# Kernel optimization log

Measured on AMD Instinct MI355X. Metric: run time of the kernel, lower is better.

## Reference

```python
import jax, jax.numpy as jnp
import numpy as np

B, G, D = 256, 14, 2048          # batch, grid, vis_embed_dim
H, A, SI, WI, ST = 1024, 512, 1024, 1024, 256  # sent_hidden, att, sent_input, word_input, int_stop
T = 10                           # max_no_of_sent


def _lin(key, out_d, in_d):
    k1, k2 = jax.random.split(key)
    return (jax.random.normal(k1, (out_d, in_d), jnp.float32) * 0.02,
            jax.random.normal(k2, (out_d,), jnp.float32) * 0.02)


def setup_inputs() -> dict:
    key = jax.random.key(0)
    ks = jax.random.split(key, 14)
    inp = {}
    inp['vis_enc_output'] = jax.random.normal(ks[0], (B, G, G, D), jnp.float32)
    inp['captions'] = jax.random.randint(ks[1], (B, T, 20), 0, 1000, jnp.int64 if jax.config.jax_enable_x64 else jnp.int32)
    inp['enc_att_w'], inp['enc_att_b'] = _lin(ks[2], A, D)
    inp['dec_att_w'], inp['dec_att_b'] = _lin(ks[3], A, H)
    inp['full_att_w'], inp['full_att_b'] = _lin(ks[4], 1, A)
    inp['ctx_w'], inp['ctx_b'] = _lin(ks[5], SI, D)
    inp['w_ih'], inp['b_ih'] = _lin(ks[6], 4 * H, SI)
    inp['w_hh'], inp['b_hh'] = _lin(ks[7], 4 * H, H)
    inp['topic_h_w'], inp['topic_h_b'] = _lin(ks[8], WI, H)
    inp['topic_c_w'], inp['topic_c_b'] = _lin(ks[9], WI, SI)
    inp['stop_p_w'], inp['stop_p_b'] = _lin(ks[10], ST, H)
    inp['stop_c_w'], inp['stop_c_b'] = _lin(ks[11], ST, H)
    inp['final_w'], inp['final_b'] = _lin(ks[12], 2, ST)
    return inp


def _forward(vis_enc_output, captions, enc_att_w, enc_att_b, dec_att_w, dec_att_b,
             full_att_w, full_att_b, ctx_w, ctx_b, w_ih, b_ih, w_hh, b_hh,
             topic_h_w, topic_h_b, topic_c_w, topic_c_b,
             stop_p_w, stop_p_b, stop_c_w, stop_c_b, final_w, final_b):
    bsz = vis_enc_output.shape[0]
    v = vis_enc_output.reshape(bsz, -1, vis_enc_output.shape[-1])  # [B, N, D]
    n_sent = captions.shape[1]
    # encoder projection is hoisted out of the loop (same math each step)
    enc_proj = jnp.einsum('bnd,ad->bna', v, enc_att_w) + enc_att_b  # [B, N, A]
    hdim = w_hh.shape[1]

    def step(carry, _):
        h, c = carry
        dec = h @ dec_att_w.T + dec_att_b                            # [B, A]
        join = jnp.tanh(enc_proj + dec[:, None, :])                  # [B, N, A]
        logits = join @ full_att_w[0] + full_att_b[0]                # [B, N]
        scores = jax.nn.softmax(logits, axis=1)
        att_out = jnp.einsum('bn,bnd->bd', scores, v)                # [B, D]
        ctx = att_out @ ctx_w.T + ctx_b                              # [B, SI]
        h_prev = h
        gates = ctx @ w_ih.T + b_ih + h @ w_hh.T + b_hh              # [B, 4H]
        i, f, g, o = jnp.split(gates, 4, axis=1)
        c_new = jax.nn.sigmoid(f) * c + jax.nn.sigmoid(i) * jnp.tanh(g)
        h_new = jax.nn.sigmoid(o) * jnp.tanh(c_new)
        topic = jnp.tanh(h_new @ topic_h_w.T + topic_h_b + ctx @ topic_c_w.T + topic_c_b)
        p = jnp.tanh(h_prev @ stop_p_w.T + stop_p_b + h_new @ stop_c_w.T + stop_c_b)
        p = p @ final_w.T + final_b                                  # [B, 2]
        return (h_new, c_new), (topic, p)

    h0 = jnp.zeros((bsz, hdim), v.dtype)
    c0 = jnp.zeros((bsz, hdim), v.dtype)
    (_, _), (topics, ps) = jax.lax.scan(step, (h0, c0), None, length=n_sent)
    return topics.transpose(1, 0, 2), ps.transpose(1, 0, 2)  # [B, T, WI], [B, T, 2]


def reference(vis_enc_output, captions, enc_att_w, enc_att_b, dec_att_w, dec_att_b,
              full_att_w, full_att_b, ctx_w, ctx_b, w_ih, b_ih, w_hh, b_hh,
              topic_h_w, topic_h_b, topic_c_w, topic_c_b,
              stop_p_w, stop_p_b, stop_c_w, stop_c_b, final_w, final_b):
    return _forward(vis_enc_output, captions, enc_att_w, enc_att_b, dec_att_w, dec_att_b,
                    full_att_w, full_att_b, ctx_w, ctx_b, w_ih, b_ih, w_hh, b_hh,
                    topic_h_w, topic_h_b, topic_c_w, topic_c_b,
                    stop_p_w, stop_p_b, stop_c_w, stop_c_b, final_w, final_b)
```

## Files before the change

kernel.cpp:

```cpp
#include <hip/hip_runtime.h>
#include <cstdint>

#define B_   256
#define NPOS 196
#define D_   2048
#define H_   1024
#define A_   512
#define T_   10

#define N13  6144
#define OFF_DEC    0
#define OFF_WHH    512
#define OFF_STOPP  4608
#define OFF_TOPICH 4864
#define OFF_STOPC  5888
#define NC   5120

#define QMAX 6.5f
#define QSINV (127.f / QMAX)
#define QS    (QMAX / 127.f)

#define PS13 ((size_t)B_ * N13)
#define PSNC ((size_t)B_ * NC)

typedef __attribute__((ext_vector_type(8))) short bf16x8;
typedef __attribute__((ext_vector_type(4))) short bf16x4;
typedef __attribute__((ext_vector_type(4))) float f32x4;

__device__ __forceinline__ float b2f(short s) {
  union { unsigned int u; float f; } c;
  c.u = ((unsigned int)(unsigned short)s) << 16;
  return c.f;
}
__device__ __forceinline__ short f2b(float f) {
  union { float f; unsigned int u; } c; c.f = f;
  unsigned int u = c.u + 0x7fffu + ((c.u >> 16) & 1u);
  return (short)(u >> 16);
}
__device__ __forceinline__ float fast_tanh(float x) {
  float a = fabsf(x);
  float e = __expf(-2.f * a);
  float t = __fdividef(1.f - e, 1.f + e);
  return x < 0.f ? -t : t;
}
__device__ __forceinline__ float fast_sigm(float x) {
  return __fdividef(1.f, 1.f + __expf(-x));
}

#define GLDS16(g, l) __builtin_amdgcn_global_load_lds( \
    (const __attribute__((address_space(1))) void*)(g), \
    (__attribute__((address_space(3))) void*)(l), 16, 0, 0)

__global__ __launch_bounds__(256) void cvtq_v_k(
    const float* __restrict__ in, short* __restrict__ v16,
    unsigned char* __restrict__ v8, long n)
{
  long i = ((long)blockIdx.x * blockDim.x + threadIdx.x) * 8;
  const long stride = (long)gridDim.x * blockDim.x * 8;
  for (; i < n; i += stride) {
    float4 a = *(const float4*)(in + i);
    float4 b = *(const float4*)(in + i + 4);
    bf16x8 o;
    o[0]=f2b(a.x); o[1]=f2b(a.y); o[2]=f2b(a.z); o[3]=f2b(a.w);
    o[4]=f2b(b.x); o[5]=f2b(b.y); o[6]=f2b(b.z); o[7]=f2b(b.w);
    *(bf16x8*)(v16 + i) = o;
    float v[8] = {a.x,a.y,a.z,a.w,b.x,b.y,b.z,b.w};
    unsigned int w0 = 0, w1 = 0;
    #pragma unroll
    for (int j = 0; j < 4; ++j) {
      float q = fminf(fmaxf(rintf(v[j] * QSINV), -127.f), 127.f) + 128.f;
      w0 |= ((unsigned int)(int)q) << (8 * j);
    }
    #pragma unroll
    for (int j = 0; j < 4; ++j) {
      float q = fminf(fmaxf(rintf(v[4+j] * QSINV), -127.f), 127.f) + 128.f;
      w1 |= ((unsigned int)(int)q) << (8 * j);
    }
    uint2 pk; pk.x = w0; pk.y = w1;
    *(uint2*)(v8 + i) = pk;
  }
}

__global__ void cvt_k(const float* __restrict__ in, short* __restrict__ out, long n)
{
  long i = ((long)blockIdx.x * blockDim.x + threadIdx.x) * 8;
  const long stride = (long)gridDim.x * blockDim.x * 8;
  for (; i < n; i += stride) {
    float4 a = *(const float4*)(in + i);
    float4 b = *(const float4*)(in + i + 4);
    bf16x8 o;
    o[0]=f2b(a.x); o[1]=f2b(a.y); o[2]=f2b(a.z); o[3]=f2b(a.w);
    o[4]=f2b(b.x); o[5]=f2b(b.y); o[6]=f2b(b.z); o[7]=f2b(b.w);
    *(bf16x8*)(out + i) = o;
  }
}

struct SegTab {
  const float* src[8];
  short* dst[8];
  int cum[9];
};
__global__ __launch_bounds__(256) void cvt_multi_k(SegTab t)
{
  int seg = 0;
  #pragma unroll
  for (int s = 0; s < 7; ++s) seg += (int)(blockIdx.x >= (unsigned)t.cum[s + 1]);
  const long i = ((long)(blockIdx.x - t.cum[seg]) * 256 + threadIdx.x) * 8;
  const float* in = t.src[seg];
  float4 a = *(const float4*)(in + i);
  float4 b = *(const float4*)(in + i + 4);
  bf16x8 o;
  o[0]=f2b(a.x); o[1]=f2b(a.y); o[2]=f2b(a.z); o[3]=f2b(a.w);
  o[4]=f2b(b.x); o[5]=f2b(b.y); o[6]=f2b(b.z); o[7]=f2b(b.w);
  *(bf16x8*)(t.dst[seg] + i) = o;
}

__global__ __launch_bounds__(256) void transpose_cvt_k(
    const float* __restrict__ in, short* __restrict__ out, int R, int C)
{
  __shared__ float t[32][33];
  const int r0 = blockIdx.y * 32, c0 = blockIdx.x * 32;
  const int tx = threadIdx.x & 31, ty = threadIdx.x >> 5;
  #pragma unroll
  for (int i = 0; i < 32; i += 8)
    t[ty + i][tx] = in[(size_t)(r0 + ty + i) * C + c0 + tx];
  __syncthreads();
  #pragma unroll
  for (int i = 0; i < 32; i += 8)
    out[(size_t)(c0 + ty + i) * R + r0 + tx] = f2b(t[tx][ty + i]);
}

__global__ __launch_bounds__(256) void biasc_k(
    const float* __restrict__ w_ih, const float* __restrict__ b_ih,
    const float* __restrict__ topic_c_w, const float* __restrict__ topic_c_b,
    const float* __restrict__ ctx_b, float* __restrict__ out)
{
  const int r = blockIdx.x * 4 + (threadIdx.x >> 6);
  const int l = threadIdx.x & 63;
  const float* wr; float bb;
  if (r < 4096) { wr = w_ih + (size_t)r * 1024;               bb = b_ih[r]; }
  else          { wr = topic_c_w + (size_t)(r - 4096) * 1024; bb = topic_c_b[r - 4096]; }
  float s = 0.f;
  #pragma unroll
  for (int k = 0; k < 16; ++k) s += wr[l + 64 * k] * ctx_b[l + 64 * k];
  #pragma unroll
  for (int o = 32; o; o >>= 1) s += __shfl_down(s, o);
  if (!l) out[r] = s + bb;
}

__global__ __launch_bounds__(256) void bias13_k(
    const float* __restrict__ dec_att_b, const float* __restrict__ b_hh,
    const float* __restrict__ stop_p_b, const float* __restrict__ topic_h_b,
    const float* __restrict__ stop_c_b, float* __restrict__ bias13)
{
  const int j = blockIdx.x * 256 + threadIdx.x;
  float v;
  if      (j < OFF_WHH)    v = dec_att_b[j];
  else if (j < OFF_STOPP)  v = b_hh[j - OFF_WHH];
  else if (j < OFF_TOPICH) v = stop_p_b[j - OFF_STOPP];
  else if (j < OFF_STOPC)  v = topic_h_b[j - OFF_TOPICH];
  else                     v = stop_c_b[j - OFF_STOPC];
  bias13[j] = v;
}

template<int OUTBF16, int BN, int SWZ, int KZ>
__global__ __launch_bounds__(256) void gemm_bt_k(
    const short* __restrict__ Aptr, const short* __restrict__ Bptr,
    const float* __restrict__ bias, void* __restrict__ Cout,
    int M, int N, int K)
{
  constexpr int TOT = 16 + BN / 8;
  constexpr int NW  = BN / 32;
  __shared__ short As[128 * 64];
  __shared__ short Bs[BN * 64];
  const int tid = threadIdx.x;
  const int l = tid & 63, wv = tid >> 6;
  const int wr = wv >> 1, wc = wv & 1;
  size_t m0, n0;
  if (SWZ) {
    const int id  = blockIdx.y * 4 + blockIdx.x;
    const int xcd = id & 7, s = id >> 3;
    m0 = (size_t)(xcd * 49 + (s >> 2)) * 128;
    n0 = (size_t)(s & 3) * BN;
  } else {
    m0 = (size_t)blockIdx.y * 128;
    n0 = (size_t)blockIdx.x * BN;
  }
  const int srow = l >> 3, scol = (l & 7) * 8;
  const int lr = l & 15, lg = l >> 4;
  const int KC = K / KZ;
  const int kbase = (KZ > 1) ? blockIdx.z * KC : 0;

  f32x4 acc[4][NW];
  #pragma unroll
  for (int i = 0; i < 4; ++i)
    #pragma unroll
    for (int j = 0; j < NW; ++j) acc[i][j] = (f32x4){0.f, 0.f, 0.f, 0.f};

  for (int k0 = kbase; k0 < kbase + KC; k0 += 64) {
    #pragma unroll
    for (int i = 0; i < TOT / 4; ++i) {
      const int c = i * 4 + wv;
      if (c < 16) {
        const int row = c * 8 + srow;
        GLDS16(Aptr + (m0 + row) * (size_t)K + k0 + scol, As + c * 512);
      } else {
        const int row = (c - 16) * 8 + srow;
        GLDS16(Bptr + (n0 + row) * (size_t)K + k0 + scol, Bs + (c - 16) * 512);
      }
    }
    __syncthreads();
    #pragma unroll
    for (int kk = 0; kk < 64; kk += 32) {
      bf16x8 af[4], bfr[NW];
      #pragma unroll
      for (int m = 0; m < 4; ++m)
        af[m] = *(const bf16x8*)(As + (wr * 64 + m * 16 + lr) * 64 + kk + lg * 8);
      #pragma unroll
      for (int n = 0; n < NW; ++n)
        bfr[n] = *(const bf16x8*)(Bs + (wc * (BN / 2) + n * 16 + lr) * 64 + kk + lg * 8);
      #pragma unroll
      for (int m = 0; m < 4; ++m)
        #pragma unroll
        for (int n = 0; n < NW; ++n)
          acc[m][n] = __builtin_amdgcn_mfma_f32_16x16x32_bf16(af[m], bfr[n], acc[m][n], 0, 0, 0);
    }
    __syncthreads();
  }

  #pragma unroll
  for (int m = 0; m < 4; ++m) {
    const size_t row = m0 + wr * 64 + m * 16 + lg * 4;
    #pragma unroll
    for (int n = 0; n < NW; ++n) {
      const size_t col = n0 + wc * (BN / 2) + n * 16 + lr;
      if (KZ > 1) {
        float* Cp = (float*)Cout + (size_t)blockIdx.z * M * (size_t)N;
        #pragma unroll
        for (int r = 0; r < 4; ++r)
          Cp[(row + r) * (size_t)N + col] = acc[m][n][r];
      } else {
        const float bv = bias[col];
        #pragma unroll
        for (int r = 0; r < 4; ++r) {
          const float v = acc[m][n][r] + bv;
          if (OUTBF16) ((short*)Cout)[(row + r) * (size_t)N + col] = f2b(v);
          else         ((float*)Cout)[(row + r) * (size_t)N + col] = v;
        }
      }
    }
  }
}

template<int DO_FINAL, int DO_SCORES>
__global__ __launch_bounds__(512) void sf_k(
    const float* __restrict__ pcur, const float* __restrict__ pprev,
    const float* __restrict__ g3p, const float* __restrict__ biasc,
    const float* __restrict__ bias13,
    const short* __restrict__ encp, const float* __restrict__ fullw,
    const float* __restrict__ finw, const float* __restrict__ finb,
    float* __restrict__ scbuf, float* __restrict__ out_t,
    float* __restrict__ out_p, int tprev)
{
  const int b = blockIdx.x, tid = threadIdx.x;
  const int l = tid & 63, wv = tid >> 6;
  const size_t b13 = (size_t)b * N13;
  __shared__ float dec_s[A_], fw_s[A_], sc[NPOS], red[16], pp[256];

  if (DO_FINAL) {
    float* ot = out_t + (size_t)b * (T_ * 1024) + (size_t)tprev * 1024;
    #pragma unroll
    for (int i = 0; i < 2; ++i) {
      const int j = tid + i * 512;
      float th = bias13[OFF_TOPICH + j] + pcur[b13 + OFF_TOPICH + j]
               + pcur[PS13 + b13 + OFF_TOPICH + j];
      float tc = biasc[4096 + j];
      #pragma unroll
      for (int z = 0; z < 4; ++z) tc += g3p[z * PSNC + (size_t)b * NC + 4096 + j];
      ot[j] = fast_tanh(th + tc);
    }
    if (tid < 256) {
      float a = bias13[OFF_STOPP + tid] + pprev[b13 + OFF_STOPP + tid]
              + pprev[PS13 + b13 + OFF_STOPP + tid];
      float c = bias13[OFF_STOPC + tid] + pcur[b13 + OFF_STOPC + tid]
              + pcur[PS13 + b13 + OFF_STOPC + tid];
      pp[tid] = fast_tanh(a + c);
    }
  }
  if (DO_SCORES && tid < A_) {
    dec_s[tid] = pcur[b13 + tid] + pcur[PS13 + b13 + tid] + bias13[tid];
    fw_s[tid]  = fullw[tid];
  }
  __syncthreads();

  if (DO_FINAL && wv < 2) {
    float s = 0.f;
    #pragma unroll
    for (int k = 0; k < 4; ++k) s += pp[l + 64 * k] * finw[wv * 256 + l + 64 * k];
    #pragma unroll
    for (int o = 32; o; o >>= 1) s += __shfl_down(s, o);
    if (!l) out_p[(size_t)b * (T_ * 2) + tprev * 2 + wv] = s + finb[wv];
  }

  if (DO_SCORES) {
    const short* ep = encp + (size_t)b * NPOS * A_;
    for (int n = wv; n < NPOS; n += 8) {
      bf16x8 e = *(const bf16x8*)(ep + (size_t)n * A_ + l * 8);
      float s = 0.f;
      #pragma unroll
      for (int j = 0; j < 8; ++j)
        s += fast_tanh(b2f(e[j]) + dec_s[l * 8 + j]) * fw_s[l * 8 + j];
      #pragma unroll
      for (int o = 32; o; o >>= 1) s += __shfl_down(s, o);
      if (!l) sc[n] = s;
    }
    __syncthreads();

    float lm = (tid < NPOS) ? sc[tid] : -3e38f;
    #pragma unroll
    for (int o = 32; o; o >>= 1) lm = fmaxf(lm, __shfl_down(lm, o));
    if (!l) red[wv] = lm;
    __syncthreads();
    float mx = red[0];
    #pragma unroll
    for (int i = 1; i < 8; ++i) mx = fmaxf(mx, red[i]);
    const float ev = (tid < NPOS) ? __expf(sc[tid] - mx) : 0.f;
    float es = ev;
    #pragma unroll
    for (int o = 32; o; o >>= 1) es += __shfl_down(es, o);
    if (!l) red[8 + wv] = es;
    __syncthreads();
    float tot = red[8];
    #pragma unroll
    for (int i = 1; i < 8; ++i) tot += red[8 + i];
    if (tid < NPOS) scbuf[(size_t)b * NPOS + tid] = ev * __fdividef(1.f, tot);
  }
}

template<int VMODE>
__global__ __launch_bounds__(256) void pv_k(
    const void* __restrict__ vptr, const float* __restrict__ scbuf,
    short* __restrict__ attout)
{
  const int b = blockIdx.y;
  const int dbase = blockIdx.x * 1024;
  const int tid = threadIdx.x;
  const int grp = tid >> 7;
  const int dt = (tid & 127) * 8;
  __shared__ float sc[NPOS];
  __shared__ float tmp[1024];
  if (tid < NPOS) sc[tid] = scbuf[(size_t)b * NPOS + tid];
  __syncthreads();

  float a[8] = {0,0,0,0,0,0,0,0};
  if (VMODE == 1) {
    const unsigned char* vb = (const unsigned char*)vptr
        + (size_t)b * NPOS * D_ + dbase + dt;
    #pragma unroll 8
    for (int n = grp; n < NPOS; n += 2) {
      const float s = sc[n];
      const uint2 w = *(const uint2*)(vb + (size_t)n * D_);
      a[0] += s * (float)(w.x & 255u);
      a[1] += s * (float)((w.x >> 8) & 255u);
      a[2] += s * (float)((w.x >> 16) & 255u);
      a[3] += s * (float)(w.x >> 24);
      a[4] += s * (float)(w.y & 255u);
      a[5] += s * (float)((w.y >> 8) & 255u);
      a[6] += s * (float)((w.y >> 16) & 255u);
      a[7] += s * (float)(w.y >> 24);
    }
  } else {
    const float* vf = (const float*)vptr + (size_t)b * NPOS * D_ + dbase + dt;
    #pragma unroll 2
    for (int n = grp; n < NPOS; n += 2) {
      const float s = sc[n];
      float4 v0 = *(const float4*)(vf + (size_t)n * D_);
      float4 v1 = *(const float4*)(vf + (size_t)n * D_ + 4);
      a[0] += s*v0.x; a[1] += s*v0.y; a[2] += s*v0.z; a[3] += s*v0.w;
      a[4] += s*v1.x; a[5] += s*v1.y; a[6] += s*v1.z; a[7] += s*v1.w;
    }
  }
  if (grp == 1) {
    #pragma unroll
    for (int j = 0; j < 8; ++j) tmp[dt + j] = a[j];
  }
  __syncthreads();
  if (grp == 0) {
    bf16x8 o8;
    #pragma unroll
    for (int j = 0; j < 8; ++j) {
      float v = a[j] + tmp[dt + j];
      if (VMODE == 1) v = v * QS - 128.f * QS;
      o8[j] = f2b(v);
    }
    *(bf16x8*)(attout + (size_t)b * D_ + dbase + dt) = o8;
  }
}

__global__ __launch_bounds__(256) void lstm_k(
    const float* __restrict__ g3p, const float* __restrict__ gPp,
    const float* __restrict__ biasc, const float* __restrict__ bias13,
    float* __restrict__ c, short* __restrict__ hbf)
{
  const int idx = (blockIdx.x * 256 + threadIdx.x) * 4;
  const int b = idx >> 10, j = idx & 1023;
  f32x4 gate[4];
  #pragma unroll
  for (int g = 0; g < 4; ++g) {
    const size_t base  = (size_t)b * NC + g * 1024 + j;
    const size_t baseh = (size_t)b * N13 + OFF_WHH + g * 1024 + j;
    f32x4 s = *(const f32x4*)(biasc + g * 1024 + j);
    s += *(const f32x4*)(bias13 + OFF_WHH + g * 1024 + j);
    #pragma unroll
    for (int z = 0; z < 4; ++z) s += *(const f32x4*)(g3p + z * PSNC + base);
    #pragma unroll
    for (int z = 0; z < 2; ++z) s += *(const f32x4*)(gPp + z * PS13 + baseh);
    gate[g] = s;
  }
  f32x4 cv = *(const f32x4*)(c + idx);
  f32x4 cn;
  bf16x4 hn;
  #pragma unroll
  for (int k = 0; k < 4; ++k) {
    const float nc2 = fast_sigm(gate[1][k]) * cv[k]
                    + fast_sigm(gate[0][k]) * fast_tanh(gate[2][k]);
    cn[k] = nc2;
    hn[k] = f2b(fast_sigm(gate[3][k]) * fast_tanh(nc2));
  }
  *(f32x4*)(c + idx) = cn;
  *(bf16x4*)(hbf + idx) = hn;
}

extern "C" void kernel_launch(void* const* d_in, const int* in_sizes, int n_in,
                              void* d_out, int out_size, void* d_ws, size_t ws_size,
                              hipStream_t stream)
{
  const float* vis       = (const float*)d_in[0];
  const float* enc_att_w = (const float*)d_in[2];
  const float* enc_att_b = (const float*)d_in[3];
  const float* dec_att_w = (const float*)d_in[4];
  const float* dec_att_b = (const float*)d_in[5];
  const float* full_att_w= (const float*)d_in[6];
  const float* ctx_w     = (const float*)d_in[8];
  const float* ctx_b     = (const float*)d_in[9];
  const float* w_ih      = (const float*)d_in[10];
  const float* b_ih      = (const float*)d_in[11];
  const float* w_hh      = (const float*)d_in[12];
  const float* b_hh      = (const float*)d_in[13];
  const float* topic_h_w = (const float*)d_in[14];
  const float* topic_h_b = (const float*)d_in[15];
  const float* topic_c_w = (const float*)d_in[16];
  const float* topic_c_b = (const float*)d_in[17];
  const float* stop_p_w  = (const float*)d_in[18];
  const float* stop_p_b  = (const float*)d_in[19];
  const float* stop_c_w  = (const float*)d_in[20];
  const float* stop_c_b  = (const float*)d_in[21];
  const float* final_w   = (const float*)d_in[22];
  const float* final_b   = (const float*)d_in[23];

  uint8_t* wsp = (uint8_t*)d_ws;
  size_t off = 0;
  auto take = [&](size_t bytes) -> void* {
    void* p = wsp + off;
    off = (off + bytes + 255) & ~(size_t)255;
    return p;
  };

  short* encproj = (short*)take((size_t)B_ * NPOS * A_ * 2);
  short* encw    = (short*)take((size_t)A_ * D_ * 2);
  short* w2cat   = (short*)take((size_t)NC * 1024 * 2);
  short* ctxwT   = (short*)take((size_t)D_ * 1024 * 2);
  short* Wc      = (short*)take((size_t)NC * D_ * 2);
  short* w13     = (short*)take((size_t)N13 * H_ * 2);
  float* biasc   = (float*)take((size_t)NC * 4);
  float* bias13  = (float*)take((size_t)N13 * 4);
  float* zeros   = (float*)take((size_t)D_ * 4);
  short* hbf     = (short*)take((size_t)B_ * H_ * 2);
  float* cst     = (float*)take((size_t)B_ * H_ * 4);
  float* pairs0  = (float*)take(2 * PS13 * 4);
  float* pairs1  = (float*)take(2 * PS13 * 4);
  float* g3p     = (float*)take(4 * PSNC * 4);
  short* attb    = (short*)take((size_t)B_ * D_ * 2);
  float* scbuf   = (float*)take((size_t)B_ * NPOS * 4);
  const size_t base0 = off;
  const long   nv = (long)B_ * NPOS * D_;
  unsigned char* v8 = (unsigned char*)take((size_t)nv);
  short* v16 = (short*)(wsp + off);
  const bool full = (ws_size >= off + (size_t)nv * 2);

  float* out_t = (float*)d_out;
  float* out_p = (float*)d_out + (size_t)B_ * T_ * 1024;

  {
    SegTab t;
    const float* srcs[8] = {enc_att_w, w_ih, topic_c_w, dec_att_w, w_hh,
                            stop_p_w, topic_h_w, stop_c_w};
    short* dsts[8] = {encw, w2cat, w2cat + (size_t)4096 * 1024,
                      w13 + (size_t)OFF_DEC * 1024, w13 + (size_t)OFF_WHH * 1024,
                      w13 + (size_t)OFF_STOPP * 1024, w13 + (size_t)OFF_TOPICH * 1024,
                      w13 + (size_t)OFF_STOPC * 1024};
    const int nel[8] = {1048576, 4194304, 1048576, 524288, 4194304, 262144, 1048576, 262144};
    int c = 0;
    for (int i = 0; i < 8; ++i) {
      t.src[i] = srcs[i]; t.dst[i] = dsts[i];
      t.cum[i] = c; c += nel[i] / 2048;
    }
    t.cum[8] = c;
    cvt_multi_k<<<c, 256, 0, stream>>>(t);
  }
  transpose_cvt_k<<<dim3(D_ / 32, 1024 / 32), 256, 0, stream>>>(ctx_w, ctxwT, 1024, D_);
  hipMemsetAsync(zeros, 0, (size_t)D_ * 4, stream);
  gemm_bt_k<1, 128, 0, 1><<<dim3(D_ / 128, NC / 128), 256, 0, stream>>>(
      w2cat, ctxwT, zeros, Wc, NC, D_, 1024);
  biasc_k<<<NC / 4, 256, 0, stream>>>(w_ih, b_ih, topic_c_w, topic_c_b, ctx_b, biasc);
  bias13_k<<<N13 / 256, 256, 0, stream>>>(
      dec_att_b, b_hh, stop_p_b, topic_h_b, stop_c_b, bias13);
  hipMemsetAsync(cst, 0, (size_t)B_ * H_ * 4, stream);
  hipMemsetAsync(pairs1, 0, 2 * PS13 * 4, stream);

  const int Mrows = B_ * NPOS;
  if (full) {
    cvtq_v_k<<<8192, 256, 0, stream>>>(vis, v16, v8, nv);
    gemm_bt_k<1, 128, 1, 1><<<dim3(A_ / 128, Mrows / 128), 256, 0, stream>>>(
        v16, encw, enc_att_b, encproj, Mrows, A_, D_);
  } else {
    const size_t avail = (ws_size > base0) ? ws_size - base0 : 0;
    int dt = 1;
    const int cand[] = {56, 28, 14, 8, 7, 4, 2, 1};
    for (int c : cand)
      if ((392 % c) == 0 && (size_t)c * 128 * D_ * 2 <= avail) { dt = c; break; }
    short* vchunk = (short*)(wsp + base0);
    const int CR = dt * 128;
    for (int s = 0; s < Mrows; s += CR) {
      cvt_k<<<4096, 256, 0, stream>>>(vis + (size_t)s * D_, vchunk, (long)CR * D_);
      gemm_bt_k<1, 128, 0, 1><<<dim3(A_ / 128, dt), 256, 0, stream>>>(
          vchunk, encw, enc_att_b, encproj + (size_t)s * A_, CR, A_, D_);
    }
  }

  for (int t = 0; t < T_; ++t) {
    float* pcur  = (t & 1) ? pairs0 : pairs1;
    float* pprev = (t & 1) ? pairs1 : pairs0;
    if (t == 0)
      sf_k<0, 1><<<B_, 512, 0, stream>>>(pcur, pprev, g3p, biasc, bias13,
          encproj, full_att_w, final_w, final_b, scbuf, out_t, out_p, 0);
    else
      sf_k<1, 1><<<B_, 512, 0, stream>>>(pcur, pprev, g3p, biasc, bias13,
          encproj, full_att_w, final_w, final_b, scbuf, out_t, out_p, t - 1);
    if (full) pv_k<1><<<dim3(2, B_), 256, 0, stream>>>(v8, scbuf, attb);
    else      pv_k<0><<<dim3(2, B_), 256, 0, stream>>>(vis, scbuf, attb);
    gemm_bt_k<0, 32, 0, 4><<<dim3(NC / 32, B_ / 128, 4), 256, 0, stream>>>(
        attb, Wc, nullptr, g3p, B_, NC, D_);
    lstm_k<<<(B_ * H_) / 1024, 256, 0, stream>>>(g3p, pcur, biasc, bias13, cst, hbf);
    float* pnew = (t & 1) ? pairs1 : pairs0;
    gemm_bt_k<0, 32, 0, 2><<<dim3(N13 / 32, B_ / 128, 2), 256, 0, stream>>>(
        hbf, w13, nullptr, pnew, B_, N13, H_);
  }
  {
    float* pcur  = ((T_ - 1) & 1) ? pairs1 : pairs0;
    float* pprev = ((T_ - 1) & 1) ? pairs0 : pairs1;
    sf_k<1, 0><<<B_, 512, 0, stream>>>(pcur, pprev, g3p, biasc, bias13,
        encproj, full_att_w, final_w, final_b, scbuf, out_t, out_p, T_ - 1);
  }
}
```

Baseline: 1.170 ms.

## Split attention scores across two blocks per batch and move softmax into pv kernel

The scores kernel now runs two blocks per batch row, each computing raw logits for 98 of the 196 positions and the matching half of the topic outputs. The softmax max/sum reduction moves into the pv kernel, which normalises the logits before the weighted sum. The point is to double parallelism in the per-step scores kernel, which had only 256 blocks. The per-step GEMMs also switch from 32-wide to 64-wide N tiles and the LSTM kernel drops to 128-thread blocks, trading block count against per-block reuse. Each pv block now repeats the softmax reduction, adding a small amount of extra work.

```diff
diff --git a/kernel.cpp b/kernel.cpp
--- a/kernel.cpp
+++ b/kernel.cpp
@@ -190,6 +190,7 @@
   const int lr = l & 15, lg = l >> 4;
   const int KC = K / KZ;
   const int kbase = (KZ > 1) ? blockIdx.z * KC : 0;
+  const int kend  = kbase + KC;
 
   f32x4 acc[4][NW];
   #pragma unroll
@@ -197,7 +198,7 @@
     #pragma unroll
     for (int j = 0; j < NW; ++j) acc[i][j] = (f32x4){0.f, 0.f, 0.f, 0.f};
 
-  for (int k0 = kbase; k0 < kbase + KC; k0 += 64) {
+  for (int k0 = kbase; k0 < kend; k0 += 64) {
     #pragma unroll
     for (int i = 0; i < TOT / 4; ++i) {
       const int c = i * 4 + wv;
@@ -253,7 +254,7 @@
 }
 
 template<int DO_FINAL, int DO_SCORES>
-__global__ __launch_bounds__(512) void sf_k(
+__global__ __launch_bounds__(512) void scores_k(
     const float* __restrict__ pcur, const float* __restrict__ pprev,
     const float* __restrict__ g3p, const float* __restrict__ biasc,
     const float* __restrict__ bias13,
@@ -262,24 +263,21 @@
     float* __restrict__ scbuf, float* __restrict__ out_t,
     float* __restrict__ out_p, int tprev)
 {
-  const int b = blockIdx.x, tid = threadIdx.x;
+  const int j = blockIdx.x, b = blockIdx.y, tid = threadIdx.x;
   const int l = tid & 63, wv = tid >> 6;
   const size_t b13 = (size_t)b * N13;
-  __shared__ float dec_s[A_], fw_s[A_], sc[NPOS], red[16], pp[256];
+  __shared__ float dec_s[A_], fw_s[A_], pp[256];
 
   if (DO_FINAL) {
     float* ot = out_t + (size_t)b * (T_ * 1024) + (size_t)tprev * 1024;
-    #pragma unroll
-    for (int i = 0; i < 2; ++i) {
-      const int j = tid + i * 512;
-      float th = bias13[OFF_TOPICH + j] + pcur[b13 + OFF_TOPICH + j]
-               + pcur[PS13 + b13 + OFF_TOPICH + j];
-      float tc = biasc[4096 + j];
-      #pragma unroll
-      for (int z = 0; z < 4; ++z) tc += g3p[z * PSNC + (size_t)b * NC + 4096 + j];
-      ot[j] = fast_tanh(th + tc);
-    }
-    if (tid < 256) {
+    const int jj = j * 512 + tid;
+    float th = bias13[OFF_TOPICH + jj] + pcur[b13 + OFF_TOPICH + jj]
+             + pcur[PS13 + b13 + OFF_TOPICH + jj];
+    float tc = biasc[4096 + jj];
+    #pragma unroll
+    for (int z = 0; z < 4; ++z) tc += g3p[z * PSNC + (size_t)b * NC + 4096 + jj];
+    ot[jj] = fast_tanh(th + tc);
+    if (j == 0 && tid < 256) {
       float a = bias13[OFF_STOPP + tid] + pprev[b13 + OFF_STOPP + tid]
               + pprev[PS13 + b13 + OFF_STOPP + tid];
       float c = bias13[OFF_STOPC + tid] + pcur[b13 + OFF_STOPC + tid]
@@ -287,13 +285,13 @@
       pp[tid] = fast_tanh(a + c);
     }
   }
-  if (DO_SCORES && tid < A_) {
+  if (DO_SCORES) {
     dec_s[tid] = pcur[b13 + tid] + pcur[PS13 + b13 + tid] + bias13[tid];
     fw_s[tid]  = fullw[tid];
   }
   __syncthreads();
 
-  if (DO_FINAL && wv < 2) {
+  if (DO_FINAL && j == 0 && wv < 2) {
     float s = 0.f;
     #pragma unroll
     for (int k = 0; k < 4; ++k) s += pp[l + 64 * k] * finw[wv * 256 + l + 64 * k];
@@ -303,37 +301,17 @@
   }
 
   if (DO_SCORES) {
-    const short* ep = encp + (size_t)b * NPOS * A_;
-    for (int n = wv; n < NPOS; n += 8) {
+    const short* ep = encp + ((size_t)b * NPOS + j * 98) * A_;
+    for (int n = wv; n < 98; n += 8) {
       bf16x8 e = *(const bf16x8*)(ep + (size_t)n * A_ + l * 8);
       float s = 0.f;
       #pragma unroll
-      for (int j = 0; j < 8; ++j)
-        s += fast_tanh(b2f(e[j]) + dec_s[l * 8 + j]) * fw_s[l * 8 + j];
+      for (int k = 0; k < 8; ++k)
+        s += fast_tanh(b2f(e[k]) + dec_s[l * 8 + k]) * fw_s[l * 8 + k];
       #pragma unroll
       for (int o = 32; o; o >>= 1) s += __shfl_down(s, o);
-      if (!l) sc[n] = s;
-    }
-    __syncthreads();
-
-    float lm = (tid < NPOS) ? sc[tid] : -3e38f;
-    #pragma unroll
-    for (int o = 32; o; o >>= 1) lm = fmaxf(lm, __shfl_down(lm, o));
-    if (!l) red[wv] = lm;
-    __syncthreads();
-    float mx = red[0];
-    #pragma unroll
-    for (int i = 1; i < 8; ++i) mx = fmaxf(mx, red[i]);
-    const float ev = (tid < NPOS) ? __expf(sc[tid] - mx) : 0.f;
-    float es = ev;
-    #pragma unroll
-    for (int o = 32; o; o >>= 1) es += __shfl_down(es, o);
-    if (!l) red[8 + wv] = es;
-    __syncthreads();
-    float tot = red[8];
-    #pragma unroll
-    for (int i = 1; i < 8; ++i) tot += red[8 + i];
-    if (tid < NPOS) scbuf[(size_t)b * NPOS + tid] = ev * __fdividef(1.f, tot);
+      if (!l) scbuf[(size_t)b * NPOS + j * 98 + n] = s;
+    }
   }
 }
 
@@ -345,13 +323,30 @@
   const int b = blockIdx.y;
   const int dbase = blockIdx.x * 1024;
   const int tid = threadIdx.x;
+  const int l = tid & 63, wvq = tid >> 6;
+  __shared__ float sc[NPOS];
+  __shared__ float red[8];
+  __shared__ float tmp[1024];
+
+  const float lg = (tid < NPOS) ? scbuf[(size_t)b * NPOS + tid] : -3e38f;
+  float lm = lg;
+  #pragma unroll
+  for (int o = 32; o; o >>= 1) lm = fmaxf(lm, __shfl_down(lm, o));
+  if (!l) red[wvq] = lm;
+  __syncthreads();
+  const float mx = fmaxf(fmaxf(red[0], red[1]), fmaxf(red[2], red[3]));
+  const float ev = (tid < NPOS) ? __expf(lg - mx) : 0.f;
+  float es = ev;
+  #pragma unroll
+  for (int o = 32; o; o >>= 1) es += __shfl_down(es, o);
+  if (!l) red[4 + wvq] = es;
+  __syncthreads();
+  const float inv = __fdividef(1.f, red[4] + red[5] + red[6] + red[7]);
+  if (tid < NPOS) sc[tid] = ev * inv;
+  __syncthreads();
+
   const int grp = tid >> 7;
   const int dt = (tid & 127) * 8;
-  __shared__ float sc[NPOS];
-  __shared__ float tmp[1024];
-  if (tid < NPOS) sc[tid] = scbuf[(size_t)b * NPOS + tid];
-  __syncthreads();
-
   float a[8] = {0,0,0,0,0,0,0,0};
   if (VMODE == 1) {
     const unsigned char* vb = (const unsigned char*)vptr
@@ -382,27 +377,27 @@
   }
   if (grp == 1) {
     #pragma unroll
-    for (int j = 0; j < 8; ++j) tmp[dt + j] = a[j];
+    for (int k = 0; k < 8; ++k) tmp[dt + k] = a[k];
   }
   __syncthreads();
   if (grp == 0) {
     bf16x8 o8;
     #pragma unroll
-    for (int j = 0; j < 8; ++j) {
-      float v = a[j] + tmp[dt + j];
+    for (int k = 0; k < 8; ++k) {
+      float v = a[k] + tmp[dt + k];
       if (VMODE == 1) v = v * QS - 128.f * QS;
-      o8[j] = f2b(v);
+      o8[k] = f2b(v);
     }
     *(bf16x8*)(attout + (size_t)b * D_ + dbase + dt) = o8;
   }
 }
 
-__global__ __launch_bounds__(256) void lstm_k(
+__global__ __launch_bounds__(128) void lstm_k(
     const float* __restrict__ g3p, const float* __restrict__ gPp,
     const float* __restrict__ biasc, const float* __restrict__ bias13,
     float* __restrict__ c, short* __restrict__ hbf)
 {
-  const int idx = (blockIdx.x * 256 + threadIdx.x) * 4;
+  const int idx = (blockIdx.x * 128 + threadIdx.x) * 4;
   const int b = idx >> 10, j = idx & 1023;
   f32x4 gate[4];
   #pragma unroll
@@ -542,24 +537,24 @@
     float* pcur  = (t & 1) ? pairs0 : pairs1;
     float* pprev = (t & 1) ? pairs1 : pairs0;
     if (t == 0)
-      sf_k<0, 1><<<B_, 512, 0, stream>>>(pcur, pprev, g3p, biasc, bias13,
+      scores_k<0, 1><<<dim3(2, B_), 512, 0, stream>>>(pcur, pprev, g3p, biasc, bias13,
           encproj, full_att_w, final_w, final_b, scbuf, out_t, out_p, 0);
     else
-      sf_k<1, 1><<<B_, 512, 0, stream>>>(pcur, pprev, g3p, biasc, bias13,
+      scores_k<1, 1><<<dim3(2, B_), 512, 0, stream>>>(pcur, pprev, g3p, biasc, bias13,
           encproj, full_att_w, final_w, final_b, scbuf, out_t, out_p, t - 1);
     if (full) pv_k<1><<<dim3(2, B_), 256, 0, stream>>>(v8, scbuf, attb);
     else      pv_k<0><<<dim3(2, B_), 256, 0, stream>>>(vis, scbuf, attb);
-    gemm_bt_k<0, 32, 0, 4><<<dim3(NC / 32, B_ / 128, 4), 256, 0, stream>>>(
+    gemm_bt_k<0, 64, 0, 4><<<dim3(NC / 64, B_ / 128, 4), 256, 0, stream>>>(
         attb, Wc, nullptr, g3p, B_, NC, D_);
-    lstm_k<<<(B_ * H_) / 1024, 256, 0, stream>>>(g3p, pcur, biasc, bias13, cst, hbf);
+    lstm_k<<<(B_ * H_) / 512, 128, 0, stream>>>(g3p, pcur, biasc, bias13, cst, hbf);
     float* pnew = (t & 1) ? pairs1 : pairs0;
-    gemm_bt_k<0, 32, 0, 2><<<dim3(N13 / 32, B_ / 128, 2), 256, 0, stream>>>(
+    gemm_bt_k<0, 64, 0, 2><<<dim3(N13 / 64, B_ / 128, 2), 256, 0, stream>>>(
         hbf, w13, nullptr, pnew, B_, N13, H_);
   }
   {
     float* pcur  = ((T_ - 1) & 1) ? pairs1 : pairs0;
     float* pprev = ((T_ - 1) & 1) ? pairs0 : pairs1;
-    sf_k<1, 0><<<B_, 512, 0, stream>>>(pcur, pprev, g3p, biasc, bias13,
+    scores_k<1, 0><<<dim3(2, B_), 512, 0, stream>>>(pcur, pprev, g3p, biasc, bias13,
         encproj, full_att_w, final_w, final_b, scbuf, out_t, out_p, T_ - 1);
   }
 }
```

Result: faster. 1.120 ms, median of 2 (-4.3%).
